# Optimization experiments

Hardware: AMD Instinct MI355X
Metric: run time of the kernel (lower is better)

The kernel has to match this reference:

```python
import jax, jax.numpy as jnp
import numpy as np

HQ, HKV, D, BS = 128, 16, 128, 128  # q heads, kv heads, head dim, block size
ROPE_BASE = 10000.0


def rope(x):
    # x: (B, S, H, D); rotate-half RoPE with cos/sin tiled to full head dim
    d = x.shape[-1]
    inv_freq = 1.0 / (ROPE_BASE ** (jnp.arange(0, d, 2, dtype=jnp.float32) / d))  # (D/2,)
    pos = jnp.arange(x.shape[1], dtype=jnp.float32)
    ang = pos[:, None] * inv_freq[None, :]                      # (S, D/2)
    cos = jnp.tile(jnp.cos(ang), (1, 2))[None, :, None, :]      # (1, S, 1, D)
    sin = jnp.tile(jnp.sin(ang), (1, 2))[None, :, None, :]
    x1, x2 = x[..., : d // 2], x[..., d // 2 :]
    x_rot = jnp.concatenate([-x2, x1], axis=-1)
    return x * cos + x_rot * sin


def setup_inputs() -> dict:
    key = jax.random.key(0)
    ks = jax.random.split(key, 5)
    s = 0.02
    E, B, S = 8192, 2, 2048
    return {
        "x": jax.random.normal(ks[0], (B, S, E), jnp.float32),
        "Wq": jax.random.normal(ks[1], (E, HQ * D), jnp.float32) * s,
        "bq": jnp.zeros((HQ * D,), jnp.float32),
        "Wk": jax.random.normal(ks[2], (E, HKV * D), jnp.float32) * s,
        "bk": jnp.zeros((HKV * D,), jnp.float32),
        "Wv": jax.random.normal(ks[3], (E, HKV * D), jnp.float32) * s,
        "bv": jnp.zeros((HKV * D,), jnp.float32),
        "Wo": jax.random.normal(ks[4], (HQ * D, E), jnp.float32) * s,
        "bo": jnp.zeros((E,), jnp.float32),
    }


def reference(x, Wq, bq, Wk, bk, Wv, bv, Wo, bo):
    B, S, E = x.shape
    G = HQ // HKV  # q heads per kv head (GQA group size) = 8
    nb = S // BS   # number of non-overlapping attention blocks

    q = (x @ Wq + bq).reshape(B, S, HQ, D)
    k = (x @ Wk + bk).reshape(B, S, HKV, D)
    v = (x @ Wv + bv).reshape(B, S, HKV, D)
    q = rope(q)
    k = rope(k)

    # Block-diagonal attention: queries only attend within their own block.
    qb = q.reshape(B, nb, BS, HKV, G, D)   # group consecutive q heads per kv head
    kb = k.reshape(B, nb, BS, HKV, D)
    vb = v.reshape(B, nb, BS, HKV, D)

    scale = 1.0 / jnp.sqrt(jnp.float32(D))
    logits = jnp.einsum('bnqhgd,bnkhd->bnhgqk', qb, kb) * scale  # (B,nb,HKV,G,BS,BS)
    attn = jax.nn.softmax(logits, axis=-1)
    ob = jnp.einsum('bnhgqk,bnkhd->bnqhgd', attn, vb)            # (B,nb,BS,HKV,G,D)
    attn_out = ob.reshape(B, S, HQ * D)

    out = attn_out @ Wo + bo
    return out, k, v
```

## Files before the change

### kernel.cpp

```cpp
#include <hip/hip_runtime.h>

typedef __attribute__((ext_vector_type(8))) short bf16x8;
typedef __attribute__((ext_vector_type(8))) unsigned short u16x8;
typedef __attribute__((ext_vector_type(4))) float f32x4;
typedef __attribute__((ext_vector_type(16))) float f32x16;

__device__ __forceinline__ unsigned short f2bf(float f){
    unsigned int u = __builtin_bit_cast(unsigned int, f);
    u += 0x7fffu + ((u >> 16) & 1u);
    return (unsigned short)(u >> 16);
}
__device__ __forceinline__ float bf2f(unsigned short h){
    unsigned int u = ((unsigned int)h) << 16;
    return __builtin_bit_cast(float, u);
}
__device__ __forceinline__ f32x4 mfma16(bf16x8 a, bf16x8 b, f32x4 c){
    return __builtin_amdgcn_mfma_f32_16x16x32_bf16(a, b, c, 0, 0, 0);
}
__device__ __forceinline__ f32x16 mfma32(bf16x8 a, bf16x8 b, f32x16 c){
    return __builtin_amdgcn_mfma_f32_32x32x16_bf16(a, b, c, 0, 0, 0);
}
__device__ __forceinline__ void gl16(const unsigned short* g, unsigned short* l){
    __builtin_amdgcn_global_load_lds(
        (const __attribute__((address_space(1))) unsigned int*)g,
        (__attribute__((address_space(3))) unsigned int*)l, 16, 0, 0);
}
#define BAR() asm volatile("s_barrier" ::: "memory")

__global__ __launch_bounds__(256) void cvt_x_kernel(const float* __restrict__ x,
                                                    unsigned short* __restrict__ xb){
    size_t i = ((size_t)blockIdx.x * 256 + threadIdx.x) * 4;
    float4 f = *(const float4*)(x + i);
    ushort4 o;
    o.x = f2bf(f.x); o.y = f2bf(f.y); o.z = f2bf(f.z); o.w = f2bf(f.w);
    *(ushort4*)(xb + i) = o;
}

__global__ __launch_bounds__(256) void tr_kernel(const float* __restrict__ W, int ldn, int col0, int K,
                                                 unsigned short* __restrict__ Wt){
    __shared__ unsigned short T[64][66];
    const int t  = threadIdx.x;
    const int k0 = blockIdx.x << 6;
    const int n0 = blockIdx.y << 6;
    #pragma unroll
    for (int i = 0; i < 4; ++i){
        const int idx = i*256 + t;
        const int r   = idx >> 4;
        const int c4  = idx & 15;
        float4 v = *(const float4*)(W + (size_t)(k0 + r)*ldn + col0 + n0 + c4*4);
        T[r][c4*4+0] = f2bf(v.x); T[r][c4*4+1] = f2bf(v.y);
        T[r][c4*4+2] = f2bf(v.z); T[r][c4*4+3] = f2bf(v.w);
    }
    __syncthreads();
    const int n  = t >> 2;
    const int ks = (t & 3) * 16;
    u16x8 o0, o1;
    #pragma unroll
    for (int j = 0; j < 8; ++j){ o0[j] = T[ks+j][n]; o1[j] = T[ks+8+j][n]; }
    unsigned short* dst = Wt + (size_t)(n0 + n)*K + k0 + ks;
    *(u16x8*)dst       = o0;
    *(u16x8*)(dst + 8) = o1;
}

#define RD_A32(MH) do { _Pragma("unroll") for (int m_=0;m_<2;++m_){           \
    const int ro_ = (wm*128 + (MH)*64 + m_*32 + l31)*64;                      \
    _Pragma("unroll") for (int k_=0;k_<4;++k_)                                \
        Af[m_][k_] = *(const bf16x8*)&S[curA + ro_ + (rdc32 ^ (k_<<4))];      \
    } } while(0)

#define RD_B32(dst, NH) do {                                                  \
    const int ro_ = (wn*64 + (NH)*32 + l31)*64;                               \
    _Pragma("unroll") for (int k_=0;k_<4;++k_)                                \
        dst[k_] = *(const bf16x8*)&S[curB + ro_ + (rdc32 ^ (k_<<4))];         \
    } while(0)

#define QUAD32(Bsrc, MH, NI) do {                                             \
    __builtin_amdgcn_s_setprio(1);                                            \
    _Pragma("unroll") for (int k_=0;k_<4;++k_){                               \
        acc2[(MH)*2+0][NI] = mfma32(Af[0][k_], Bsrc[k_], acc2[(MH)*2+0][NI]); \
        acc2[(MH)*2+1][NI] = mfma32(Af[1][k_], Bsrc[k_], acc2[(MH)*2+1][NI]); \
    }                                                                         \
    __builtin_amdgcn_s_setprio(0);                                            \
} while(0)

template<int EPI>
__global__ __launch_bounds__(512, 2) void gemm256_kernel(
    const unsigned short* __restrict__ A, int K,
    const unsigned short* __restrict__ Bt, int n_off,
    const float* __restrict__ bq, const float* __restrict__ bk_,
    const float* __restrict__ bv_, const float* __restrict__ bo_,
    unsigned short* __restrict__ q_ws,
    float* __restrict__ k_out, float* __restrict__ v_out,
    unsigned short* __restrict__ v_ws,
    float* __restrict__ outp)
{
    __shared__ unsigned short S[65536];

    const int t    = threadIdx.x;
    const int lane = t & 63;
    const int wid  = t >> 6;
    const int wm   = wid >> 2, wn = wid & 3;
    const int l31  = lane & 31;
    const int wslot = wid * 512;
    const int rdswz = ((l31 & 1) << 5) | (((l31 >> 1) & 1) << 4) | (((l31 >> 2) & 1) << 3);
    const int rdc32 = ((lane >> 5) << 3) ^ rdswz;

    const int j  = blockIdx.x & 7;
    const int w  = blockIdx.x >> 3;
    const int tm = (j & 3) * 4 + (w & 3);
    const int tn = (j >> 2) * 8 + (w >> 2);
    const int brow  = tm * 256;
    const int nbase = tn * 256;
    const int gcol0 = n_off + nbase;

    const int scol = ((t & 7) * 8) ^ (((t >> 5) & 1) << 3) ^ (((t >> 4) & 1) << 4) ^ (((t >> 3) & 1) << 5);
    const int srow = t >> 3;
    const unsigned short* pA0 = A  + (size_t)(brow  + srow)*K + scol;
    const unsigned short* pA1 = pA0 + (size_t)128*K;
    const unsigned short* pB0 = Bt + (size_t)(nbase + srow)*K + scol;
    const unsigned short* pB1 = pB0 + (size_t)128*K;

    auto stage = [&](const unsigned short* gb, int ktt, int ldsoff){
        const unsigned short* g0 = gb + (size_t)ktt * 64;
        gl16(g0,                 &S[ldsoff + wslot]);
        gl16(g0 + (size_t)64*K,  &S[ldsoff + wslot + 4096]);
    };

    f32x16 acc2[4][2];
    #pragma unroll
    for (int i = 0; i < 4; ++i)
        #pragma unroll
        for (int jj = 0; jj < 2; ++jj)
            #pragma unroll
            for (int e = 0; e < 16; ++e) acc2[i][jj][e] = 0.f;

    bf16x8 Af[2][4], Bf0[4], Bf1[4];
    const int NT = K >> 6;

    stage(pB0, 0, 16384);
    stage(pA0, 0, 0);
    stage(pA1, 0, 8192);
    stage(pB1, 0, 24576);
    stage(pB0, 1, 32768 + 16384);
    stage(pA0, 1, 32768);
    asm volatile("s_waitcnt vmcnt(4)" ::: "memory");
    BAR();

    for (int kt = 0; kt < NT; ++kt){
        const int cur = kt & 1, nxt = cur ^ 1;
        const int curA = cur * 32768, curB = curA + 16384;
        const int nxtA = nxt * 32768, nxtB = nxtA + 16384;

        RD_A32(0); RD_B32(Bf0, 0);
        if (kt + 1 < NT) stage(pA1, kt + 1, nxtA + 8192);
        BAR();
        QUAD32(Bf0, 0, 0);

        RD_B32(Bf1, 1);
        if (kt + 1 < NT) stage(pB1, kt + 1, nxtB + 8192);
        BAR();
        QUAD32(Bf1, 0, 1);

        RD_A32(1);
        if (kt + 2 < NT) stage(pB0, kt + 2, curB);
        BAR();
        QUAD32(Bf1, 1, 1);

        if (kt + 2 < NT){
            stage(pA0, kt + 2, curA);
            asm volatile("s_waitcnt vmcnt(4)" ::: "memory");
        } else {
            asm volatile("s_waitcnt vmcnt(0)" ::: "memory");
        }
        BAR();
        QUAD32(Bf0, 1, 0);
    }

    const int rbase = 4 * (lane >> 5);
    #pragma unroll
    for (int mi = 0; mi < 4; ++mi){
        #pragma unroll
        for (int ni = 0; ni < 2; ++ni){
            const int col = gcol0 + wn*64 + ni*32 + l31;
            int region;
            if (EPI == 1)          region = 3;
            else if (col < 16384)  region = 0;
            else if (col < 18432)  region = 1;
            else                   region = 2;
            float bias;
            if (region == 3)      bias = bo_[col];
            else if (region == 0) bias = bq[col];
            else if (region == 1) bias = bk_[col - 16384];
            else                  bias = bv_[col - 18432];
            const int row0 = brow + wm*128 + mi*32 + rbase;
            #pragma unroll
            for (int r = 0; r < 16; ++r){
                const float val = acc2[mi][ni][r] + bias;
                const size_t rr = (size_t)(row0 + (r & 3) + 8*(r >> 2));
                if (region == 3){
                    outp[rr * 8192 + col] = val;
                } else if (region == 0){
                    q_ws[rr * 16384 + col] = f2bf(val);
                } else if (region == 1){
                    k_out[rr * 2048 + (col - 16384)] = val;
                } else {
                    v_out[rr * 2048 + (col - 18432)] = val;
                    v_ws[rr * 2048 + (col - 18432)]  = f2bf(val);
                }
            }
        }
    }
}

__global__ __launch_bounds__(256) void rope_q_kernel(unsigned short* __restrict__ q){
    const size_t idx = (size_t)blockIdx.x * 256 + threadIdx.x;
    const int i = (int)(idx & 63);
    const int h = (int)((idx >> 6) & 127);
    const int r = (int)(idx >> 13);
    const int s = r & 2047;
    const float inv = exp2f(-(float)i * 0.20762050593046014f);
    float c, sn;
    sincosf((float)s * inv, &sn, &c);
    unsigned short* p = q + (size_t)r * 16384 + h * 128 + i;
    const float v1 = bf2f(p[0]);
    const float v2 = bf2f(p[64]);
    p[0]  = f2bf(v1 * c - v2 * sn);
    p[64] = f2bf(v2 * c + v1 * sn);
}

__global__ __launch_bounds__(256) void rope_k_kernel(float* __restrict__ kio,
                                                     unsigned short* __restrict__ kws){
    const size_t idx = (size_t)blockIdx.x * 256 + threadIdx.x;
    const int i = (int)(idx & 63);
    const int h = (int)((idx >> 6) & 15);
    const int r = (int)(idx >> 10);
    const int s = r & 2047;
    const float inv = exp2f(-(float)i * 0.20762050593046014f);
    float c, sn;
    sincosf((float)s * inv, &sn, &c);
    float* p = kio + (size_t)r * 2048 + h * 128 + i;
    const float v1 = p[0], v2 = p[64];
    const float o1 = v1 * c - v2 * sn;
    const float o2 = v2 * c + v1 * sn;
    p[0] = o1; p[64] = o2;
    unsigned short* pw = kws + (size_t)r * 2048 + h * 128 + i;
    pw[0]  = f2bf(o1);
    pw[64] = f2bf(o2);
}

__global__ __launch_bounds__(256) void attn_kernel(
    const unsigned short* __restrict__ q,
    const unsigned short* __restrict__ kbf,
    const unsigned short* __restrict__ vbf,
    unsigned short* __restrict__ ao)
{
    __shared__ unsigned short KV[128][136];
    __shared__ unsigned short Pls[4][16][136];

    const int t    = threadIdx.x;
    const int lane = t & 63;
    const int wid  = t >> 6;
    const int llo  = lane & 15, lhi = lane >> 4;

    const int bid = blockIdx.x;
    const int qh  = bid & 1;
    const int g   = (bid >> 1) & 7;
    const int hkv = (bid >> 4) & 15;
    const int blk = (bid >> 8) & 15;
    const int b   = bid >> 12;

    const int h     = hkv * 8 + g;
    const int sbase = b * 2048 + blk * 128;
    const int qbase = sbase + qh * 64 + wid * 16;

    {
        const int row = t >> 1;
        const int d0  = (t & 1) * 64;
        const unsigned short* src = kbf + (size_t)(sbase + row) * 2048 + hkv * 128 + d0;
        #pragma unroll
        for (int i2 = 0; i2 < 8; ++i2)
            *(int4*)&KV[row][d0 + i2*8] = *(const int4*)(src + i2*8);
    }

    bf16x8 qf[4];
    {
        const unsigned short* qp = q + (size_t)(qbase + llo) * 16384 + h * 128 + lhi * 8;
        #pragma unroll
        for (int kc = 0; kc < 4; ++kc)
            qf[kc] = *(const bf16x8*)(qp + kc * 32);
    }

    __syncthreads();

    const f32x4 zero = {0.f,0.f,0.f,0.f};
    f32x4 sc[8];
    #pragma unroll
    for (int ni = 0; ni < 8; ++ni) sc[ni] = zero;
    #pragma unroll
    for (int kc = 0; kc < 4; ++kc){
        #pragma unroll
        for (int ni = 0; ni < 8; ++ni){
            bf16x8 kf = *(const bf16x8*)&KV[ni*16 + llo][kc*32 + lhi*8];
            sc[ni] = mfma16(qf[kc], kf, sc[ni]);
        }
    }

    const float scale = 0.08838834764831845f;
    #pragma unroll
    for (int r = 0; r < 4; ++r){
        float m = sc[0][r];
        #pragma unroll
        for (int ni = 1; ni < 8; ++ni) m = fmaxf(m, sc[ni][r]);
        #pragma unroll
        for (int off = 1; off < 16; off <<= 1) m = fmaxf(m, __shfl_xor(m, off));
        float sum = 0.f;
        #pragma unroll
        for (int ni = 0; ni < 8; ++ni){
            const float p = __expf((sc[ni][r] - m) * scale);
            sc[ni][r] = p; sum += p;
        }
        #pragma unroll
        for (int off = 1; off < 16; off <<= 1) sum += __shfl_xor(sum, off);
        const float rs = 1.f / sum;
        #pragma unroll
        for (int ni = 0; ni < 8; ++ni) sc[ni][r] *= rs;
    }

    #pragma unroll
    for (int ni = 0; ni < 8; ++ni)
        #pragma unroll
        for (int r = 0; r < 4; ++r)
            Pls[wid][lhi*4 + r][ni*16 + llo] = f2bf(sc[ni][r]);

    __syncthreads();

    {
        const int d  = t & 127;
        const int j0 = (t >> 7) * 64;
        const unsigned short* vs = vbf + (size_t)sbase * 2048 + hkv * 128 + d;
        #pragma unroll
        for (int jj = 0; jj < 64; jj += 8){
            u16x8 pk;
            #pragma unroll
            for (int e = 0; e < 8; ++e)
                pk[e] = vs[(size_t)(j0 + jj + e) * 2048];
            *(u16x8*)&KV[d][j0 + jj] = pk;
        }
    }

    __syncthreads();

    f32x4 oc[8];
    #pragma unroll
    for (int ni = 0; ni < 8; ++ni) oc[ni] = zero;
    #pragma unroll
    for (int kc = 0; kc < 4; ++kc){
        bf16x8 pf = *(const bf16x8*)&Pls[wid][llo][kc*32 + lhi*8];
        #pragma unroll
        for (int ni = 0; ni < 8; ++ni){
            bf16x8 vf = *(const bf16x8*)&KV[ni*16 + llo][kc*32 + lhi*8];
            oc[ni] = mfma16(pf, vf, oc[ni]);
        }
    }

    #pragma unroll
    for (int ni = 0; ni < 8; ++ni){
        #pragma unroll
        for (int r = 0; r < 4; ++r){
            const size_t row = (size_t)(qbase + lhi*4 + r);
            ao[row * 16384 + h*128 + ni*16 + llo] = f2bf(oc[ni][r]);
        }
    }
}

extern "C" void kernel_launch(void* const* d_in, const int* in_sizes, int n_in,
                              void* d_out, int out_size, void* d_ws, size_t ws_size,
                              hipStream_t stream)
{
    const float* x  = (const float*)d_in[0];
    const float* Wq = (const float*)d_in[1];
    const float* bq = (const float*)d_in[2];
    const float* Wk = (const float*)d_in[3];
    const float* bk = (const float*)d_in[4];
    const float* Wv = (const float*)d_in[5];
    const float* bv = (const float*)d_in[6];
    const float* Wo = (const float*)d_in[7];
    const float* bo = (const float*)d_in[8];

    float* outp  = (float*)d_out;
    float* k_out = outp + (size_t)33554432;
    float* v_out = outp + (size_t)41943040;

    char* w = (char*)d_ws;
    unsigned short* xb  = (unsigned short*)(w);
    unsigned short* kb2 = (unsigned short*)(w + 67108864ull);
    unsigned short* vb2 = (unsigned short*)(w + 83886080ull);
    unsigned short* qb  = (unsigned short*)(w + 100663296ull);
    unsigned short* Wt  = (unsigned short*)(w + 234881024ull);

    cvt_x_kernel<<<32768, 256, 0, stream>>>(x, xb);

    for (int c = 0; c < 4; ++c){
        tr_kernel<<<dim3(128, 64), 256, 0, stream>>>(Wq, 16384, c*4096, 8192, Wt);
        gemm256_kernel<0><<<256, 512, 0, stream>>>(xb, 8192, Wt, c*4096, bq, bk, bv, nullptr,
                                                   qb, k_out, v_out, vb2, nullptr);
    }
    tr_kernel<<<dim3(128, 32), 256, 0, stream>>>(Wk, 2048, 0, 8192, Wt);
    tr_kernel<<<dim3(128, 32), 256, 0, stream>>>(Wv, 2048, 0, 8192, Wt + (size_t)2048*8192);
    gemm256_kernel<0><<<256, 512, 0, stream>>>(xb, 8192, Wt, 16384, bq, bk, bv, nullptr,
                                               qb, k_out, v_out, vb2, nullptr);

    rope_q_kernel<<<131072, 256, 0, stream>>>(qb);
    rope_k_kernel<<<16384, 256, 0, stream>>>(k_out, kb2);
    attn_kernel<<<8192, 256, 0, stream>>>(qb, kb2, vb2, qb);

    for (int hh = 0; hh < 2; ++hh){
        tr_kernel<<<dim3(256, 64), 256, 0, stream>>>(Wo, 8192, hh*4096, 16384, Wt);
        gemm256_kernel<1><<<256, 512, 0, stream>>>(qb, 16384, Wt, hh*4096, nullptr, nullptr, nullptr, bo,
                                                   nullptr, nullptr, nullptr, nullptr, outp);
    }
}
```

Baseline: 2.723 ms.

## Fuse Q RoPE into attention load and merge GEMM loop barriers

Removes the standalone Q RoPE kernel and applies the rotation in registers right after the attention kernel loads Q fragments. This avoids a full read-modify-write pass over the bf16 Q workspace. The GEMM main loop now has two barriers per K-step instead of four: both B halves are read and two stages are issued together, and setprio wraps pairs of MFMA groups. In exchange, register pressure rises and the attention kernel recomputes sincos, and fewer barriers may reduce overlap between LDS staging and MFMA work.

```diff
diff --git a/kernel.cpp b/kernel.cpp
--- a/kernel.cpp
+++ b/kernel.cpp
@@ -75,12 +75,10 @@
     } while(0)
 
 #define QUAD32(Bsrc, MH, NI) do {                                             \
-    __builtin_amdgcn_s_setprio(1);                                            \
     _Pragma("unroll") for (int k_=0;k_<4;++k_){                               \
         acc2[(MH)*2+0][NI] = mfma32(Af[0][k_], Bsrc[k_], acc2[(MH)*2+0][NI]); \
         acc2[(MH)*2+1][NI] = mfma32(Af[1][k_], Bsrc[k_], acc2[(MH)*2+1][NI]); \
     }                                                                         \
-    __builtin_amdgcn_s_setprio(0);                                            \
 } while(0)
 
 template<int EPI>
@@ -151,29 +149,30 @@
         const int curA = cur * 32768, curB = curA + 16384;
         const int nxtA = nxt * 32768, nxtB = nxtA + 16384;
 
-        RD_A32(0); RD_B32(Bf0, 0);
-        if (kt + 1 < NT) stage(pA1, kt + 1, nxtA + 8192);
+        RD_A32(0); RD_B32(Bf0, 0); RD_B32(Bf1, 1);
+        if (kt + 1 < NT){
+            stage(pA1, kt + 1, nxtA + 8192);
+            stage(pB1, kt + 1, nxtB + 8192);
+        }
         BAR();
+        __builtin_amdgcn_s_setprio(1);
         QUAD32(Bf0, 0, 0);
-
-        RD_B32(Bf1, 1);
-        if (kt + 1 < NT) stage(pB1, kt + 1, nxtB + 8192);
-        BAR();
         QUAD32(Bf1, 0, 1);
+        __builtin_amdgcn_s_setprio(0);
 
         RD_A32(1);
-        if (kt + 2 < NT) stage(pB0, kt + 2, curB);
-        BAR();
-        QUAD32(Bf1, 1, 1);
-
         if (kt + 2 < NT){
+            stage(pB0, kt + 2, curB);
             stage(pA0, kt + 2, curA);
             asm volatile("s_waitcnt vmcnt(4)" ::: "memory");
         } else {
             asm volatile("s_waitcnt vmcnt(0)" ::: "memory");
         }
         BAR();
+        __builtin_amdgcn_s_setprio(1);
+        QUAD32(Bf1, 1, 1);
         QUAD32(Bf0, 1, 0);
+        __builtin_amdgcn_s_setprio(0);
     }
 
     const int rbase = 4 * (lane >> 5);
@@ -212,22 +211,6 @@
     }
 }
 
-__global__ __launch_bounds__(256) void rope_q_kernel(unsigned short* __restrict__ q){
-    const size_t idx = (size_t)blockIdx.x * 256 + threadIdx.x;
-    const int i = (int)(idx & 63);
-    const int h = (int)((idx >> 6) & 127);
-    const int r = (int)(idx >> 13);
-    const int s = r & 2047;
-    const float inv = exp2f(-(float)i * 0.20762050593046014f);
-    float c, sn;
-    sincosf((float)s * inv, &sn, &c);
-    unsigned short* p = q + (size_t)r * 16384 + h * 128 + i;
-    const float v1 = bf2f(p[0]);
-    const float v2 = bf2f(p[64]);
-    p[0]  = f2bf(v1 * c - v2 * sn);
-    p[64] = f2bf(v2 * c + v1 * sn);
-}
-
 __global__ __launch_bounds__(256) void rope_k_kernel(float* __restrict__ kio,
                                                      unsigned short* __restrict__ kws){
     const size_t idx = (size_t)blockIdx.x * 256 + threadIdx.x;
@@ -289,6 +272,23 @@
         for (int kc = 0; kc < 4; ++kc)
             qf[kc] = *(const bf16x8*)(qp + kc * 32);
     }
+    {
+        const float sp = (float)((qbase + llo) & 2047);
+        #pragma unroll
+        for (int half = 0; half < 2; ++half){
+            #pragma unroll
+            for (int e = 0; e < 8; ++e){
+                const int i = half*32 + lhi*8 + e;
+                const float inv = exp2f(-(float)i * 0.20762050593046014f);
+                float sn, c;
+                sincosf(sp * inv, &sn, &c);
+                const float v1 = bf2f((unsigned short)qf[half][e]);
+                const float v2 = bf2f((unsigned short)qf[half+2][e]);
+                qf[half][e]   = (short)f2bf(v1*c - v2*sn);
+                qf[half+2][e] = (short)f2bf(v2*c + v1*sn);
+            }
+        }
+    }
 
     __syncthreads();
 
@@ -410,7 +410,6 @@
     gemm256_kernel<0><<<256, 512, 0, stream>>>(xb, 8192, Wt, 16384, bq, bk, bv, nullptr,
                                                qb, k_out, v_out, vb2, nullptr);
 
-    rope_q_kernel<<<131072, 256, 0, stream>>>(qb);
     rope_k_kernel<<<16384, 256, 0, stream>>>(k_out, kb2);
     attn_kernel<<<8192, 256, 0, stream>>>(qb, kb2, vb2, qb);
 
```

New measurement: 2.672 ms. About the same (-1.9%).
